# Kernel tuning notes

Measured on AMD Instinct MI355X. Metric: run time of the kernel, lower is better.

## Reference

```python
import jax, jax.numpy as jnp
import numpy as np

ATTN_SCALE = 0.12  # attn_args.attn_scale (constant hyperparameter)
EPS = 1e-6         # F.rms_norm eps
GATE_IN = 12       # attn_gate input features (x[..., :12])


def rms_norm(x):
    return x * jax.lax.rsqrt(jnp.mean(x * x, axis=-1, keepdims=True) + EPS)


def rotary(x, cos, sin):
    # x: [B,T,H,D]; cos/sin: [T,D//2]
    x1, x2 = jnp.split(x, 2, axis=-1)
    c = cos[None, :, None, :]
    s = sin[None, :, None, :]
    return jnp.concatenate([x1 * c + x2 * s, -x1 * s + x2 * c], axis=-1)


def setup_inputs() -> dict:
    key = jax.random.key(0)
    ks = jax.random.split(key, 5)
    B, T, D, H, HD = 1, 2048, 1024, 8, 128
    std = 0.5 * D ** -0.5
    x = jax.random.normal(ks[0], (B, T, D), jnp.float32)
    qkvo_w = jax.random.normal(ks[1], (4, D, D), jnp.float32) * std
    gate_w = jax.random.normal(ks[2], (H, GATE_IN), jnp.float32) * 0.02
    ve = jax.random.normal(ks[3], (B, T, H, HD), jnp.float32)
    sa_lambdas = jax.random.uniform(ks[4], (2,), jnp.float32, 0.3, 0.7)
    half = HD // 2
    inv_freq = 1.0 / (10000.0 ** (jnp.arange(half, dtype=jnp.float32) / half))
    ang = jnp.arange(T, dtype=jnp.float32)[:, None] * inv_freq[None, :]
    return dict(x=x, qkvo_w=qkvo_w, gate_w=gate_w, ve=ve,
                sa_lambdas=sa_lambdas, cos=jnp.cos(ang), sin=jnp.sin(ang))


def reference(x, qkvo_w, gate_w, ve, sa_lambdas, cos, sin):
    B, T, D = x.shape
    H = gate_w.shape[0]
    HD = D // H
    # fused QKV projection: rows of qkvo_w[:3] are [q; k; v]
    w_qkv = qkvo_w[:3].reshape(3 * D, D)           # [3D, D]
    qkv = jnp.einsum('btd,ed->bte', x, w_qkv)      # [B,T,3D]
    qkv = qkv.reshape(B, T, 3, H, HD)
    q, k, v = qkv[:, :, 0], qkv[:, :, 1], qkv[:, :, 2]
    # RMSNorm + RoPE on q, k
    q = rotary(rms_norm(q), cos, sin)
    k = rotary(rms_norm(k), cos, sin)
    # value-residual mixing
    v = sa_lambdas[0] * v + sa_lambdas[1] * ve
    # causal SDPA with custom scale
    scores = jnp.einsum('bqhd,bkhd->bhqk', q, k) * ATTN_SCALE
    causal = jnp.tril(jnp.ones((T, T), dtype=bool))
    scores = jnp.where(causal[None, None], scores, jnp.finfo(scores.dtype).min)
    p = jax.nn.softmax(scores, axis=-1)
    y = jnp.einsum('bhqk,bkhd->bqhd', p, v)        # [B,T,H,HD]
    # per-head sigmoid gate from the first 12 channels of x
    gate = jax.nn.sigmoid(jnp.einsum('bti,hi->bth', x[..., :GATE_IN], gate_w))
    y = y * gate[..., None]
    # output projection (qkvo_w[3]): F.linear -> y @ W_o^T
    out = jnp.einsum('bti,oi->bto', y.reshape(B, T, H * HD), qkvo_w[3])
    return out
```

## Files before the change

### kernel.cpp

```cpp
#include <hip/hip_runtime.h>
#include <stdint.h>

typedef unsigned short u16;
typedef unsigned int u32;

typedef __bf16 bfx8 __attribute__((ext_vector_type(8)));
typedef float fx4 __attribute__((ext_vector_type(4)));
typedef float fx16 __attribute__((ext_vector_type(16)));
typedef u16 u16x4 __attribute__((ext_vector_type(4)));
typedef u16 u16x8 __attribute__((ext_vector_type(8)));

#define GAS __attribute__((address_space(1)))
#define LAS __attribute__((address_space(3)))

__device__ __forceinline__ void gload16(const void* g, void* l) {
  __builtin_amdgcn_global_load_lds((GAS void*)g, (LAS void*)l, 16, 0, 0);
}

__device__ __forceinline__ u16 f2bf(float f) {
  union { float f; u32 u; } v; v.f = f;
  u32 r = v.u + 0x7fffu + ((v.u >> 16) & 1u);
  return (u16)(r >> 16);
}
__device__ __forceinline__ float bf2f(u16 u) {
  union { u32 u; float f; } v; v.u = ((u32)u) << 16;
  return v.f;
}

__device__ __forceinline__ int segF(int qb) { return (qb * qb + 2 * qb + (qb & 1)) >> 2; }

__global__ __launch_bounds__(256) void k_cvt(const float* __restrict__ src, u16* __restrict__ dst, int n) {
  int i = (blockIdx.x * 256 + threadIdx.x) * 8;
  if (i >= n) return;
  const float4* s = (const float4*)(src + i);
  float4 a = s[0], b = s[1];
  u16x8 o;
  o[0] = f2bf(a.x); o[1] = f2bf(a.y); o[2] = f2bf(a.z); o[3] = f2bf(a.w);
  o[4] = f2bf(b.x); o[5] = f2bf(b.y); o[6] = f2bf(b.z); o[7] = f2bf(b.w);
  *(u16x8*)(dst + i) = o;
}

__global__ __launch_bounds__(256) void k_gemm_out(const u16* __restrict__ A, const u16* __restrict__ B,
                                                  float* __restrict__ C, int M, int N, int K) {
  __shared__ char sm[32768];
  const int tid = threadIdx.x;
  const int l = tid & 63, w = tid >> 6;
  const int li = l & 15, lg = l >> 4;
  const int bid = (blockIdx.x & 7) * 64 + (blockIdx.x >> 3);
  const int nbm = M >> 6;
  const int bm = bid % nbm, bn = bid / nbm;

  const u16* gsrc[4];
#pragma unroll
  for (int i = 0; i < 4; ++i) {
    int b = i * 4096 + tid * 16;
    int row, ch;
    const u16* mat;
    if (b < 8192) { row = b >> 7; mat = A + (size_t)(bm * 64 + row) * K; }
    else          { int bb = b - 8192; row = bb >> 7; mat = B + (size_t)(bn * 64 + row) * K; }
    ch = ((b >> 4) & 7) ^ (row & 7);
    gsrc[i] = mat + ch * 8;
  }

  fx4 acc[4];
#pragma unroll
  for (int jj = 0; jj < 4; ++jj)
#pragma unroll
    for (int r = 0; r < 4; ++r) acc[jj][r] = 0.f;

#pragma unroll
  for (int i = 0; i < 4; ++i) gload16(gsrc[i], sm + i * 4096 + w * 1024);
  __syncthreads();
  int cur = 0;

  for (int k0 = 0; k0 < K; k0 += 64) {
    if (k0 + 64 < K) {
      char* dst = sm + (cur ^ 1) * 16384;
#pragma unroll
      for (int i = 0; i < 4; ++i) gload16(gsrc[i] + k0 + 64, dst + i * 4096 + w * 1024);
    }
    const char* base = sm + cur * 16384;
#pragma unroll
    for (int kk = 0; kk < 2; ++kk) {
      int rowa = w * 16 + li;
      bfx8 af = *(const bfx8*)(base + rowa * 128 + (((kk * 4 + lg)) ^ (rowa & 7)) * 16);
#pragma unroll
      for (int nf = 0; nf < 4; ++nf) {
        int rowb = nf * 16 + li;
        bfx8 bfr = *(const bfx8*)(base + 8192 + rowb * 128 + ((kk * 4 + lg) ^ (rowb & 7)) * 16);
        acc[nf] = __builtin_amdgcn_mfma_f32_16x16x32_bf16(af, bfr, acc[nf], 0, 0, 0);
      }
    }
    __syncthreads();
    cur ^= 1;
  }
#pragma unroll
  for (int nf = 0; nf < 4; ++nf)
#pragma unroll
    for (int r = 0; r < 4; ++r) {
      int row = bm * 64 + w * 16 + lg * 4 + r;
      int col = bn * 64 + nf * 16 + li;
      C[(size_t)row * N + col] = acc[nf][r];
    }
}

__global__ __launch_bounds__(256) void k_gemm_qkv(const u16* __restrict__ A, const u16* __restrict__ B,
                                                  u16* __restrict__ qb2, u16* __restrict__ kt2,
                                                  u16* __restrict__ vt2,
                                                  const float* __restrict__ ve, const float* __restrict__ lam,
                                                  const float* __restrict__ cosp, const float* __restrict__ sinp) {
  __shared__ char sm[49152];
  const int tid = threadIdx.x;
  const int l = tid & 63, w = tid >> 6;
  const int li = l & 15, lg = l >> 4;
  const int bid = (blockIdx.x & 7) * 96 + (blockIdx.x >> 3);
  const int bm = bid & 31, bn = bid >> 5;
  const int K = 1024;

  const u16* gsrc[6];
#pragma unroll
  for (int i = 0; i < 6; ++i) {
    int b = i * 4096 + tid * 16;
    int row, ch;
    const u16* mat;
    if (b < 8192) { row = b >> 7; mat = A + (size_t)(bm * 64 + row) * K; }
    else          { int bb = b - 8192; row = bb >> 7; mat = B + (size_t)(bn * 128 + row) * K; }
    ch = ((b >> 4) & 7) ^ (row & 7);
    gsrc[i] = mat + ch * 8;
  }

  fx4 acc[8];
#pragma unroll
  for (int jj = 0; jj < 8; ++jj)
#pragma unroll
    for (int r = 0; r < 4; ++r) acc[jj][r] = 0.f;

#pragma unroll
  for (int i = 0; i < 6; ++i) gload16(gsrc[i], sm + i * 4096 + w * 1024);
  __syncthreads();
  int cur = 0;

  for (int k0 = 0; k0 < K; k0 += 64) {
    if (k0 + 64 < K) {
      char* dst = sm + (cur ^ 1) * 24576;
#pragma unroll
      for (int i = 0; i < 6; ++i) gload16(gsrc[i] + k0 + 64, dst + i * 4096 + w * 1024);
    }
    const char* base = sm + cur * 24576;
#pragma unroll
    for (int kk = 0; kk < 2; ++kk) {
      int rowa = w * 16 + li;
      bfx8 af = *(const bfx8*)(base + rowa * 128 + ((kk * 4 + lg) ^ (rowa & 7)) * 16);
#pragma unroll
      for (int nf = 0; nf < 8; ++nf) {
        int rowb = nf * 16 + li;
        bfx8 bfr = *(const bfx8*)(base + 8192 + rowb * 128 + ((kk * 4 + lg) ^ (rowb & 7)) * 16);
        acc[nf] = __builtin_amdgcn_mfma_f32_16x16x32_bf16(af, bfr, acc[nf], 0, 0, 0);
      }
    }
    __syncthreads();
    cur ^= 1;
  }

  const int s = bn >> 3, h = bn & 7;
  if (s < 2) {
#pragma unroll
    for (int r = 0; r < 4; ++r) {
      int t = bm * 64 + w * 16 + lg * 4 + r;
      float ss = 0.f;
#pragma unroll
      for (int nf = 0; nf < 8; ++nf) ss += acc[nf][r] * acc[nf][r];
      ss += __shfl_xor(ss, 1); ss += __shfl_xor(ss, 2);
      ss += __shfl_xor(ss, 4); ss += __shfl_xor(ss, 8);
      float rn = rsqrtf(ss * (1.f / 128.f) + 1e-6f);
#pragma unroll
      for (int nf = 0; nf < 4; ++nf) {
        int dp = nf * 16 + li;
        float c = cosp[(size_t)t * 64 + dp];
        float sn = sinp[(size_t)t * 64 + dp];
        float x1 = acc[nf][r] * rn, x2 = acc[nf + 4][r] * rn;
        u16 o1 = f2bf(x1 * c + x2 * sn);
        u16 o2 = f2bf(-x1 * sn + x2 * c);
        if (s == 0) {
          u16* qp = qb2 + (size_t)t * 1024 + h * 128;
          qp[dp] = o1;
          qp[dp + 64] = o2;
        } else {
          u16* kp = kt2 + (size_t)h * 262144 + (size_t)(t >> 5) * 4096 + (t & 31) * 128;
          int dq = dp + 64;
          kp[(((dp >> 3) ^ (t & 7)) << 3) | (dp & 7)] = o1;
          kp[(((dq >> 3) ^ (t & 7)) << 3) | (dq & 7)] = o2;
        }
      }
    }
  } else {
    const float l0 = lam[0], l1 = lam[1];
    int tb = bm * 64 + w * 16 + lg * 4;
    u16* vbase = vt2 + (size_t)h * 262144 + (size_t)(tb >> 5) * 4096 + ((tb & 31) >> 3) * 1024 + (tb & 7);
#pragma unroll
    for (int nf = 0; nf < 8; ++nf) {
      int d = nf * 16 + li;
      u16x4 o;
#pragma unroll
      for (int r = 0; r < 4; ++r)
        o[r] = f2bf(l0 * acc[nf][r] + l1 * ve[(size_t)(tb + r) * 1024 + h * 128 + d]);
      *(u16x4*)(vbase + d * 8) = o;
    }
  }
}

__global__ __launch_bounds__(256) void k_attn2(const u16* __restrict__ qb2, const u16* __restrict__ kt2,
                                               const u16* __restrict__ vt2,
                                               u16* __restrict__ part, float* __restrict__ ml) {
  __shared__ char sm[49152];
  const int bid = (blockIdx.x & 7) * 72 + (blockIdx.x >> 3);
  const int h = bid / 72;
  const int r72 = bid % 72;
  int qb = 15;
  while (segF(qb) > r72) --qb;
  const int s = r72 - segF(qb);
  const int q0 = qb * 128;
  const int seg0 = s * 256;
  const int seg_len = min(256, (qb + 1) * 128 - seg0);
  const int nkt = seg_len >> 5;

  const int tid = threadIdx.x;
  const int l = tid & 63, w = tid >> 6;
  const int li = l & 31, hi = l >> 5;
  const int qrow = q0 + w * 32 + li;
  const int wqmax = q0 + w * 32 + 31;
  const int wqmin = q0 + w * 32;

  bfx8 Q[8];
  {
    const u16* qp = qb2 + (size_t)qrow * 1024 + h * 128 + hi * 8;
#pragma unroll
    for (int c = 0; c < 8; ++c) Q[c] = *(const bfx8*)(qp + c * 16);
  }

  const u16* ktile = kt2 + (size_t)h * 262144 + (size_t)(seg0 >> 5) * 4096;
  const u16* vtile = vt2 + (size_t)h * 262144 + (size_t)(seg0 >> 5) * 4096;

  auto STAGE = [&](int kt, int buf) {
    char* dst = sm + buf * 16384;
    const u16* ks = ktile + (size_t)kt * 4096;
    const u16* vs = vtile + (size_t)kt * 4096;
#pragma unroll
    for (int i = 0; i < 2; ++i) {
      int j = w * 2 + i;
      gload16(ks + j * 512 + l * 8, dst + j * 1024);
      gload16(vs + j * 512 + l * 8, dst + 8192 + j * 1024);
    }
  };

  fx16 Y[4];
#pragma unroll
  for (int d = 0; d < 4; ++d)
#pragma unroll
    for (int r = 0; r < 16; ++r) Y[d][r] = 0.f;
  float l_run = 0.f;

  STAGE(0, 0);
  STAGE(1, 1);

  for (int kt = 0; kt < nkt; ++kt) {
    asm volatile("s_waitcnt vmcnt(4)\n\ts_barrier" ::: "memory");
    if (kt + 2 < nkt) STAGE(kt + 2, (kt + 2) % 3);
    const int k0 = seg0 + kt * 32;
    if (k0 <= wqmax) {
      const char* kb = sm + (kt % 3) * 16384;
      const char* vb = kb + 8192;
      fx16 S;
#pragma unroll
      for (int r = 0; r < 16; ++r) S[r] = 0.f;
#pragma unroll
      for (int c = 0; c < 8; ++c) {
        int ch = (c * 2 + hi) ^ (li & 7);
        bfx8 kf = *(const bfx8*)(kb + li * 256 + ch * 16);
        S = __builtin_amdgcn_mfma_f32_32x32x16_bf16(kf, Q[c], S, 0, 0, 0);
      }
      const bool nomask = (k0 + 31 <= wqmin);
      float p[16];
      float ssum = 0.f;
      if (nomask) {
#pragma unroll
        for (int r = 0; r < 16; ++r) {
          float e = __expf(fmaf(S[r], 0.12f, -16.f));
          p[r] = e; ssum += e;
        }
      } else {
#pragma unroll
        for (int r = 0; r < 16; ++r) {
          int kk = (r & 3) + 8 * (r >> 2) + 4 * hi;
          float e = (k0 + kk <= qrow) ? __expf(fmaf(S[r], 0.12f, -16.f)) : 0.f;
          p[r] = e; ssum += e;
        }
      }
      ssum += __shfl_xor(ssum, 32);
      l_run += ssum;
      u32 pk[8], pks[8];
#pragma unroll
      for (int i = 0; i < 8; ++i) pk[i] = (u32)f2bf(p[2 * i]) | ((u32)f2bf(p[2 * i + 1]) << 16);
#pragma unroll
      for (int i = 0; i < 8; ++i) pks[i] = (u32)__shfl_xor((int)pk[i], 32);
      union { u32 u[4]; bfx8 v; } P0, P1;
      if (hi == 0) {
        P0.u[0] = pk[0];  P0.u[1] = pk[1];  P0.u[2] = pks[0]; P0.u[3] = pks[1];
        P1.u[0] = pk[4];  P1.u[1] = pk[5];  P1.u[2] = pks[4]; P1.u[3] = pks[5];
      } else {
        P0.u[0] = pks[2]; P0.u[1] = pks[3]; P0.u[2] = pk[2];  P0.u[3] = pk[3];
        P1.u[0] = pks[6]; P1.u[1] = pks[7]; P1.u[2] = pk[6];  P1.u[3] = pk[7];
      }
#pragma unroll
      for (int db = 0; db < 4; ++db) {
        int dd = db * 32 + li;
        bfx8 v0 = *(const bfx8*)(vb + hi * 2048 + dd * 16);
        bfx8 v1 = *(const bfx8*)(vb + (2 + hi) * 2048 + dd * 16);
        Y[db] = __builtin_amdgcn_mfma_f32_32x32x16_bf16(v0, P0.v, Y[db], 0, 0, 0);
        Y[db] = __builtin_amdgcn_mfma_f32_32x32x16_bf16(v1, P1.v, Y[db], 0, 0, 0);
      }
    }
  }
  __syncthreads();

  if (hi == 0) ml[(size_t)bid * 128 + w * 32 + li] = l_run;
  float* Yl = (float*)(sm + w * 8192);
  u16* pdst = part + (size_t)bid * 16384;
#pragma unroll
  for (int P = 0; P < 2; ++P) {
    asm volatile("" ::: "memory");
#pragma unroll
    for (int dh = 0; dh < 2; ++dh) {
      int db = P * 2 + dh;
#pragma unroll
      for (int r = 0; r < 16; ++r) {
        int dloc = dh * 32 + (r & 3) + 8 * (r >> 2) + 4 * hi;
        Yl[li * 64 + (dloc ^ ((li & 7) << 2))] = Y[db][r];
      }
    }
    asm volatile("" ::: "memory");
    int rr = l >> 1, c0 = (l & 1) * 32, sx = (rr & 7) << 2;
#pragma unroll
    for (int j = 0; j < 8; ++j) {
      float4 v = *(const float4*)(Yl + rr * 64 + ((c0 + j * 4) ^ sx));
      u16x4 o;
      o[0] = f2bf(v.x); o[1] = f2bf(v.y); o[2] = f2bf(v.z); o[3] = f2bf(v.w);
      *(u16x4*)(pdst + (w * 32 + rr) * 128 + P * 64 + c0 + j * 4) = o;
    }
  }
}

__global__ __launch_bounds__(256) void k_comb(const u16* __restrict__ part, const float* __restrict__ ml,
                                              const float* __restrict__ x, const float* __restrict__ gw,
                                              u16* __restrict__ y) {
  const int b = blockIdx.x;
  const int h = b >> 4, qb = b & 15;
  const int nseg = (qb + 2) >> 1;
  const int slot0 = h * 72 + segF(qb);
  const int t = threadIdx.x;
  const int r = t >> 1, hf = (t & 1) * 64;
  const int q = qb * 128 + r;

  float L = 0.f;
#pragma unroll
  for (int s = 0; s < 8; ++s)
    if (s < nseg) L += ml[(size_t)(slot0 + s) * 128 + r];

  float accv[64];
#pragma unroll
  for (int j = 0; j < 64; ++j) accv[j] = 0.f;
#pragma unroll
  for (int s = 0; s < 8; ++s) {
    if (s < nseg) {
      const u16x8* P = (const u16x8*)(part + (size_t)(slot0 + s) * 16384 + r * 128 + hf);
#pragma unroll
      for (int j = 0; j < 8; ++j) {
        u16x8 v = P[j];
#pragma unroll
        for (int e = 0; e < 8; ++e) accv[j * 8 + e] += bf2f(v[e]);
      }
    }
  }
  float dot = 0.f;
#pragma unroll
  for (int i = 0; i < 12; ++i) dot += x[(size_t)q * 1024 + i] * gw[h * 12 + i];
  float gt_ = 1.f / (1.f + __expf(-dot));
  float sc = gt_ / L;
  u16* yp = y + (size_t)q * 1024 + h * 128 + hf;
#pragma unroll
  for (int j = 0; j < 8; ++j) {
    u16x8 o;
#pragma unroll
    for (int e = 0; e < 8; ++e) o[e] = f2bf(accv[j * 8 + e] * sc);
    *(u16x8*)(yp + j * 8) = o;
  }
}

extern "C" void kernel_launch(void* const* d_in, const int* in_sizes, int n_in,
                              void* d_out, int out_size, void* d_ws, size_t ws_size,
                              hipStream_t stream) {
  const float* x = (const float*)d_in[0];
  const float* qkvo_w = (const float*)d_in[1];
  const float* gate_w = (const float*)d_in[2];
  const float* ve = (const float*)d_in[3];
  const float* lam = (const float*)d_in[4];
  const float* cosp = (const float*)d_in[5];
  const float* sinp = (const float*)d_in[6];
  float* out = (float*)d_out;

  u16* wb  = (u16*)d_ws;
  u16* xb  = wb + 4u * 1024 * 1024;
  u16* qb2 = xb + 2u * 1024 * 1024;
  u16* kt2 = qb2 + 2u * 1024 * 1024;
  u16* vt2 = kt2 + 2u * 1024 * 1024;
  u16* y   = vt2 + 2u * 1024 * 1024;
  u16* part = y + 2u * 1024 * 1024;
  float* ml = (float*)(part + (size_t)576 * 16384);

  k_cvt<<<dim3(2048), dim3(256), 0, stream>>>(qkvo_w, wb, 4 * 1024 * 1024);
  k_cvt<<<dim3(1024), dim3(256), 0, stream>>>(x, xb, 2 * 1024 * 1024);
  k_gemm_qkv<<<dim3(32 * 24), dim3(256), 0, stream>>>(xb, wb, qb2, kt2, vt2, ve, lam, cosp, sinp);
  k_attn2<<<dim3(576), dim3(256), 0, stream>>>(qb2, kt2, vt2, part, ml);
  k_comb<<<dim3(128), dim3(256), 0, stream>>>(part, ml, x, gate_w, y);
  k_gemm_out<<<dim3(32 * 16), dim3(256), 0, stream>>>(y, wb + 3u * 1024 * 1024, out, 2048, 1024, 1024);
}
```

Before: 95.38 us.

## Merge conversion launches, use 2-wave QKV GEMM blocks, add MFMA priority hints

The two fp32-to-bf16 conversion kernels become a single launch that covers both buffers, which saves one kernel launch. The QKV GEMM now runs 128-thread blocks, each wave computing two 16-row M fragments, so every B fragment read from LDS feeds two MFMAs. This doubles per-wave accumulators and halves the waves available per tile to hide latency. The attention kernel wraps its MFMA sections in s_setprio to favour matrix issue over other waves' softmax work.

```diff
diff --git a/kernel.cpp b/kernel.cpp
--- a/kernel.cpp
+++ b/kernel.cpp
@@ -29,15 +29,23 @@
 
 __device__ __forceinline__ int segF(int qb) { return (qb * qb + 2 * qb + (qb & 1)) >> 2; }
 
-__global__ __launch_bounds__(256) void k_cvt(const float* __restrict__ src, u16* __restrict__ dst, int n) {
+__global__ __launch_bounds__(256) void k_cvt2(const float* __restrict__ sa, u16* __restrict__ da, int na,
+                                              const float* __restrict__ sb, u16* __restrict__ db, int nb) {
   int i = (blockIdx.x * 256 + threadIdx.x) * 8;
-  if (i >= n) return;
-  const float4* s = (const float4*)(src + i);
-  float4 a = s[0], b = s[1];
+  const float* s;
+  u16* d;
+  if (i < na) { s = sa + i; d = da + i; }
+  else {
+    int j = i - na;
+    if (j >= nb) return;
+    s = sb + j; d = db + j;
+  }
+  const float4* sp = (const float4*)s;
+  float4 a = sp[0], b = sp[1];
   u16x8 o;
   o[0] = f2bf(a.x); o[1] = f2bf(a.y); o[2] = f2bf(a.z); o[3] = f2bf(a.w);
   o[4] = f2bf(b.x); o[5] = f2bf(b.y); o[6] = f2bf(b.z); o[7] = f2bf(b.w);
-  *(u16x8*)(dst + i) = o;
+  *(u16x8*)d = o;
 }
 
 __global__ __launch_bounds__(256) void k_gemm_out(const u16* __restrict__ A, const u16* __restrict__ B,
@@ -104,7 +112,7 @@
     }
 }
 
-__global__ __launch_bounds__(256) void k_gemm_qkv(const u16* __restrict__ A, const u16* __restrict__ B,
+__global__ __launch_bounds__(128) void k_gemm_qkv(const u16* __restrict__ A, const u16* __restrict__ B,
                                                   u16* __restrict__ qb2, u16* __restrict__ kt2,
                                                   u16* __restrict__ vt2,
                                                   const float* __restrict__ ve, const float* __restrict__ lam,
@@ -117,10 +125,10 @@
   const int bm = bid & 31, bn = bid >> 5;
   const int K = 1024;
 
-  const u16* gsrc[6];
-#pragma unroll
-  for (int i = 0; i < 6; ++i) {
-    int b = i * 4096 + tid * 16;
+  const u16* gsrc[12];
+#pragma unroll
+  for (int i = 0; i < 12; ++i) {
+    int b = i * 2048 + w * 1024 + l * 16;
     int row, ch;
     const u16* mat;
     if (b < 8192) { row = b >> 7; mat = A + (size_t)(bm * 64 + row) * K; }
@@ -129,14 +137,16 @@
     gsrc[i] = mat + ch * 8;
   }
 
-  fx4 acc[8];
-#pragma unroll
-  for (int jj = 0; jj < 8; ++jj)
-#pragma unroll
-    for (int r = 0; r < 4; ++r) acc[jj][r] = 0.f;
-
-#pragma unroll
-  for (int i = 0; i < 6; ++i) gload16(gsrc[i], sm + i * 4096 + w * 1024);
+  fx4 acc[2][8];
+#pragma unroll
+  for (int mf = 0; mf < 2; ++mf)
+#pragma unroll
+    for (int jj = 0; jj < 8; ++jj)
+#pragma unroll
+      for (int r = 0; r < 4; ++r) acc[mf][jj][r] = 0.f;
+
+#pragma unroll
+  for (int i = 0; i < 12; ++i) gload16(gsrc[i], sm + i * 2048 + w * 1024);
   __syncthreads();
   int cur = 0;
 
@@ -144,18 +154,23 @@
     if (k0 + 64 < K) {
       char* dst = sm + (cur ^ 1) * 24576;
 #pragma unroll
-      for (int i = 0; i < 6; ++i) gload16(gsrc[i] + k0 + 64, dst + i * 4096 + w * 1024);
+      for (int i = 0; i < 12; ++i) gload16(gsrc[i] + k0 + 64, dst + i * 2048 + w * 1024);
     }
     const char* base = sm + cur * 24576;
 #pragma unroll
     for (int kk = 0; kk < 2; ++kk) {
-      int rowa = w * 16 + li;
-      bfx8 af = *(const bfx8*)(base + rowa * 128 + ((kk * 4 + lg) ^ (rowa & 7)) * 16);
+      bfx8 af[2];
+#pragma unroll
+      for (int mf = 0; mf < 2; ++mf) {
+        int rowa = w * 32 + mf * 16 + li;
+        af[mf] = *(const bfx8*)(base + rowa * 128 + ((kk * 4 + lg) ^ (rowa & 7)) * 16);
+      }
 #pragma unroll
       for (int nf = 0; nf < 8; ++nf) {
         int rowb = nf * 16 + li;
         bfx8 bfr = *(const bfx8*)(base + 8192 + rowb * 128 + ((kk * 4 + lg) ^ (rowb & 7)) * 16);
-        acc[nf] = __builtin_amdgcn_mfma_f32_16x16x32_bf16(af, bfr, acc[nf], 0, 0, 0);
+        acc[0][nf] = __builtin_amdgcn_mfma_f32_16x16x32_bf16(af[0], bfr, acc[0][nf], 0, 0, 0);
+        acc[1][nf] = __builtin_amdgcn_mfma_f32_16x16x32_bf16(af[1], bfr, acc[1][nf], 0, 0, 0);
       }
     }
     __syncthreads();
@@ -165,46 +180,51 @@
   const int s = bn >> 3, h = bn & 7;
   if (s < 2) {
 #pragma unroll
-    for (int r = 0; r < 4; ++r) {
-      int t = bm * 64 + w * 16 + lg * 4 + r;
-      float ss = 0.f;
-#pragma unroll
-      for (int nf = 0; nf < 8; ++nf) ss += acc[nf][r] * acc[nf][r];
-      ss += __shfl_xor(ss, 1); ss += __shfl_xor(ss, 2);
-      ss += __shfl_xor(ss, 4); ss += __shfl_xor(ss, 8);
-      float rn = rsqrtf(ss * (1.f / 128.f) + 1e-6f);
-#pragma unroll
-      for (int nf = 0; nf < 4; ++nf) {
-        int dp = nf * 16 + li;
-        float c = cosp[(size_t)t * 64 + dp];
-        float sn = sinp[(size_t)t * 64 + dp];
-        float x1 = acc[nf][r] * rn, x2 = acc[nf + 4][r] * rn;
-        u16 o1 = f2bf(x1 * c + x2 * sn);
-        u16 o2 = f2bf(-x1 * sn + x2 * c);
-        if (s == 0) {
-          u16* qp = qb2 + (size_t)t * 1024 + h * 128;
-          qp[dp] = o1;
-          qp[dp + 64] = o2;
-        } else {
-          u16* kp = kt2 + (size_t)h * 262144 + (size_t)(t >> 5) * 4096 + (t & 31) * 128;
-          int dq = dp + 64;
-          kp[(((dp >> 3) ^ (t & 7)) << 3) | (dp & 7)] = o1;
-          kp[(((dq >> 3) ^ (t & 7)) << 3) | (dq & 7)] = o2;
+    for (int mf = 0; mf < 2; ++mf)
+#pragma unroll
+      for (int r = 0; r < 4; ++r) {
+        int t = bm * 64 + w * 32 + mf * 16 + lg * 4 + r;
+        float ss = 0.f;
+#pragma unroll
+        for (int nf = 0; nf < 8; ++nf) ss += acc[mf][nf][r] * acc[mf][nf][r];
+        ss += __shfl_xor(ss, 1); ss += __shfl_xor(ss, 2);
+        ss += __shfl_xor(ss, 4); ss += __shfl_xor(ss, 8);
+        float rn = rsqrtf(ss * (1.f / 128.f) + 1e-6f);
+#pragma unroll
+        for (int nf = 0; nf < 4; ++nf) {
+          int dp = nf * 16 + li;
+          float c = cosp[(size_t)t * 64 + dp];
+          float sn = sinp[(size_t)t * 64 + dp];
+          float x1 = acc[mf][nf][r] * rn, x2 = acc[mf][nf + 4][r] * rn;
+          u16 o1 = f2bf(x1 * c + x2 * sn);
+          u16 o2 = f2bf(-x1 * sn + x2 * c);
+          if (s == 0) {
+            u16* qp = qb2 + (size_t)t * 1024 + h * 128;
+            qp[dp] = o1;
+            qp[dp + 64] = o2;
+          } else {
+            u16* kp = kt2 + (size_t)h * 262144 + (size_t)(t >> 5) * 4096 + (t & 31) * 128;
+            int dq = dp + 64;
+            kp[(((dp >> 3) ^ (t & 7)) << 3) | (dp & 7)] = o1;
+            kp[(((dq >> 3) ^ (t & 7)) << 3) | (dq & 7)] = o2;
+          }
         }
       }
-    }
   } else {
     const float l0 = lam[0], l1 = lam[1];
-    int tb = bm * 64 + w * 16 + lg * 4;
-    u16* vbase = vt2 + (size_t)h * 262144 + (size_t)(tb >> 5) * 4096 + ((tb & 31) >> 3) * 1024 + (tb & 7);
-#pragma unroll
-    for (int nf = 0; nf < 8; ++nf) {
-      int d = nf * 16 + li;
-      u16x4 o;
-#pragma unroll
-      for (int r = 0; r < 4; ++r)
-        o[r] = f2bf(l0 * acc[nf][r] + l1 * ve[(size_t)(tb + r) * 1024 + h * 128 + d]);
-      *(u16x4*)(vbase + d * 8) = o;
+#pragma unroll
+    for (int mf = 0; mf < 2; ++mf) {
+      int tb = bm * 64 + w * 32 + mf * 16 + lg * 4;
+      u16* vbase = vt2 + (size_t)h * 262144 + (size_t)(tb >> 5) * 4096 + ((tb & 31) >> 3) * 1024 + (tb & 7);
+#pragma unroll
+      for (int nf = 0; nf < 8; ++nf) {
+        int d = nf * 16 + li;
+        u16x4 o;
+#pragma unroll
+        for (int r = 0; r < 4; ++r)
+          o[r] = f2bf(l0 * acc[mf][nf][r] + l1 * ve[(size_t)(tb + r) * 1024 + h * 128 + d]);
+        *(u16x4*)(vbase + d * 8) = o;
+      }
     }
   }
 }
@@ -273,12 +293,14 @@
       fx16 S;
 #pragma unroll
       for (int r = 0; r < 16; ++r) S[r] = 0.f;
+      __builtin_amdgcn_s_setprio(1);
 #pragma unroll
       for (int c = 0; c < 8; ++c) {
         int ch = (c * 2 + hi) ^ (li & 7);
         bfx8 kf = *(const bfx8*)(kb + li * 256 + ch * 16);
         S = __builtin_amdgcn_mfma_f32_32x32x16_bf16(kf, Q[c], S, 0, 0, 0);
       }
+      __builtin_amdgcn_s_setprio(0);
       const bool nomask = (k0 + 31 <= wqmin);
       float p[16];
       float ssum = 0.f;
@@ -311,6 +333,7 @@
         P0.u[0] = pks[2]; P0.u[1] = pks[3]; P0.u[2] = pk[2];  P0.u[3] = pk[3];
         P1.u[0] = pks[6]; P1.u[1] = pks[7]; P1.u[2] = pk[6];  P1.u[3] = pk[7];
       }
+      __builtin_amdgcn_s_setprio(1);
 #pragma unroll
       for (int db = 0; db < 4; ++db) {
         int dd = db * 32 + li;
@@ -319,6 +342,7 @@
         Y[db] = __builtin_amdgcn_mfma_f32_32x32x16_bf16(v0, P0.v, Y[db], 0, 0, 0);
         Y[db] = __builtin_amdgcn_mfma_f32_32x32x16_bf16(v1, P1.v, Y[db], 0, 0, 0);
       }
+      __builtin_amdgcn_s_setprio(0);
     }
   }
   __syncthreads();
@@ -417,9 +441,8 @@
   u16* part = y + 2u * 1024 * 1024;
   float* ml = (float*)(part + (size_t)576 * 16384);
 
-  k_cvt<<<dim3(2048), dim3(256), 0, stream>>>(qkvo_w, wb, 4 * 1024 * 1024);
-  k_cvt<<<dim3(1024), dim3(256), 0, stream>>>(x, xb, 2 * 1024 * 1024);
-  k_gemm_qkv<<<dim3(32 * 24), dim3(256), 0, stream>>>(xb, wb, qb2, kt2, vt2, ve, lam, cosp, sinp);
+  k_cvt2<<<dim3(3072), dim3(256), 0, stream>>>(qkvo_w, wb, 4 * 1024 * 1024, x, xb, 2 * 1024 * 1024);
+  k_gemm_qkv<<<dim3(32 * 24), dim3(128), 0, stream>>>(xb, wb, qb2, kt2, vt2, ve, lam, cosp, sinp);
   k_attn2<<<dim3(576), dim3(256), 0, stream>>>(qb2, kt2, vt2, part, ml);
   k_comb<<<dim3(128), dim3(256), 0, stream>>>(part, ml, x, gate_w, y);
   k_gemm_out<<<dim3(32 * 16), dim3(256), 0, stream>>>(y, wb + 3u * 1024 * 1024, out, 2048, 1024, 1024);
```

New measurement: 96.13 us. About the same (+0.8%).
